# Optimization experiments

Hardware: AMD Instinct MI355X
Metric: run time of the kernel (lower is better)

## Reference

```python
import jax, jax.numpy as jnp
import numpy as np

LN2 = 0.6931471805599453

def ssp(x):
    # 'shifted_sp' activation: softplus(x) - log(2)
    return jax.nn.softplus(x) - LN2

def _res_chain(x, W1, b1, W2, b2):
    # PhysNetResidual chain: x <- lin2(ssp(lin1(ssp(x)))) + x
    # W1/W2: [n_res, F, F], b1/b2: [n_res, F]
    for j in range(W1.shape[0]):
        h = ssp(x) @ W1[j] + b1[j]
        x = ssp(h) @ W2[j] + b2[j] + x
    return x

def _physnet_module(feat, radial_aev, idx12, p):
    (W_I, b_I, W_J, b_J, W_gate, gvec, W_int, b_int,
     ri_W1, ri_b1, ri_W2, ri_b2,
     ra_W1, ra_b1, ra_W2, ra_b2,
     ro_W1, ro_b1, ro_W2, ro_b2, W_out, b_out) = p
    N, F = feat.shape
    # self term (no species are dummy -> non_dummy indexing is identity)
    h_self = ssp(ssp(feat) @ W_I + b_I)                       # [N,F]
    # pair messages
    gate = radial_aev @ W_gate                                 # [P,F] (no bias)
    f12 = feat[idx12]                                          # [2,P,F] gather
    fm = ssp(ssp(f12) @ W_J + b_J)                             # [2,P,F]
    pair_msg = gate[None] * fm                                 # [2,P,F]
    proto = jnp.zeros_like(feat).at[idx12.reshape(-1)].add(
        pair_msg.reshape(-1, F))                               # scatter-add
    proto = proto + h_self
    msg = _res_chain(proto, ri_W1, ri_b1, ri_W2, ri_b2)
    feat2 = feat * gvec + ssp(msg) @ W_int + b_int
    feat2 = _res_chain(feat2, ra_W1, ra_b1, ra_W2, ra_b2)
    e = ssp(_res_chain(feat2, ro_W1, ro_b1, ro_W2, ro_b2)) @ W_out + b_out  # [N]
    return e, feat2

def setup_inputs() -> dict:
    key = jax.random.key(0)
    L, F, R = 5, 128, 64
    M, A = 128, 64
    N = M * A
    P = 400000
    ks = jax.random.split(key, 20)
    s = 0.05  # small weight scale keeps activations stable across 5 modules
    inp = {
        'species': jax.random.randint(ks[0], (M, A), 0, 4, dtype=jnp.int32),
        'features': jax.random.normal(ks[1], (N, F), jnp.float32),
        'radial_aev': jax.random.uniform(ks[2], (P, R), jnp.float32),
        'atom_index12': jax.random.randint(ks[3], (2, P), 0, N, dtype=jnp.int32),
        'W_I': jax.random.normal(ks[4], (L, F, F)) * s,
        'b_I': jnp.zeros((L, F)),
        'W_J': jax.random.normal(ks[5], (L, F, F)) * s,
        'b_J': jnp.zeros((L, F)),
        'W_gate': jax.random.normal(ks[6], (L, R, F)) * s,
        'gvec': jnp.ones((L, F)),
        'W_int': jax.random.normal(ks[7], (L, F, F)) * s,
        'b_int': jnp.zeros((L, F)),
        'ri_W1': jax.random.normal(ks[8], (L, 3, F, F)) * s,
        'ri_b1': jnp.zeros((L, 3, F)),
        'ri_W2': jax.random.normal(ks[9], (L, 3, F, F)) * s,
        'ri_b2': jnp.zeros((L, 3, F)),
        'ra_W1': jax.random.normal(ks[10], (L, 2, F, F)) * s,
        'ra_b1': jnp.zeros((L, 2, F)),
        'ra_W2': jax.random.normal(ks[11], (L, 2, F, F)) * s,
        'ra_b2': jnp.zeros((L, 2, F)),
        'ro_W1': jax.random.normal(ks[12], (L, 1, F, F)) * s,
        'ro_b1': jnp.zeros((L, 1, F)),
        'ro_W2': jax.random.normal(ks[13], (L, 1, F, F)) * s,
        'ro_b2': jnp.zeros((L, 1, F)),
        'W_out': jax.random.normal(ks[14], (L, F)) * s,
        'b_out': jnp.zeros((L,)),
    }
    return inp

def reference(species, features, radial_aev, atom_index12,
              W_I, b_I, W_J, b_J, W_gate, gvec, W_int, b_int,
              ri_W1, ri_b1, ri_W2, ri_b2,
              ra_W1, ra_b1, ra_W2, ra_b2,
              ro_W1, ro_b1, ro_W2, ro_b2, W_out, b_out):
    M, A = species.shape
    params = (W_I, b_I, W_J, b_J, W_gate, gvec, W_int, b_int,
              ri_W1, ri_b1, ri_W2, ri_b2,
              ra_W1, ra_b1, ra_W2, ra_b2,
              ro_W1, ro_b1, ro_W2, ro_b2, W_out, b_out)
    feat = features
    energies = jnp.zeros((M * A,), features.dtype)
    for l in range(W_I.shape[0]):  # fixed small module loop
        p = tuple(arr[l] for arr in params)
        e, feat = _physnet_module(feat, radial_aev, atom_index12, p)
        energies = energies + e
    return energies.reshape(M, A), feat
```

## Files before the change

kernel.cpp:

```cpp
#include <hip/hip_runtime.h>


#define LN2F 0.69314718055994530942f
#define NB 128

using short8  = __attribute__((ext_vector_type(8))) short;
using float4v = __attribute__((ext_vector_type(4))) float;

__device__ __forceinline__ float sspf(float x) {
  float ax = fabsf(x);
  return fmaxf(x, 0.0f) + __logf(1.0f + __expf(-ax)) - LN2F;
}

__device__ __forceinline__ unsigned short f2bf(float x) {
  return (unsigned short)((__float_as_uint(x) + 0x8000u) >> 16);
}

__device__ __forceinline__ unsigned short f2bf_ne(float x) {
  unsigned int u = __float_as_uint(x);
  u += 0x7fffu + ((u >> 16) & 1u);
  return (unsigned short)(u >> 16);
}

struct K1Args {
  const float* wsrc[80];
  int isgate[80];
  const float* bp[17];
  int bstride[17];
  const float* b_out;
  const int* idx;
  unsigned short* Wt;
  float* bias_pack;
  unsigned int* H;
  int n2p, C;
};

__global__ __launch_bounds__(256) void k1_prep(K1Args K) {
  __shared__ unsigned int h[8192];
  int b = blockIdx.x, tid = threadIdx.x;
  if (b < 80) {
    const float* s = K.wsrc[b];
    unsigned short* d = K.Wt + (size_t)b * 16384;
    if (!K.isgate[b]) {
      for (int it = 0; it < 8; ++it) {
        int id = tid + it * 256;
        int lane = id & 63, mm = (id >> 6) & 3, c8 = id >> 8;
        int l16 = lane & 15, quad = lane >> 4;
        int n = 16 * c8 + l16, k0 = 8 * (4 * mm + quad);
        unsigned short tmp[8];
#pragma unroll
        for (int cc = 0; cc < 8; ++cc) tmp[cc] = f2bf_ne(s[(k0 + cc) * 128 + n]);
        *(uint4*)(d + c8 * 2048 + mm * 512 + lane * 8) = *(uint4*)tmp;
      }
    } else {
      for (int it = 0; it < 4; ++it) {
        int id = tid + it * 256;
        int lane = id & 63, mm = (id >> 6) & 1, c8 = id >> 7;
        int l16 = lane & 15, quad = lane >> 4;
        int n = 16 * c8 + l16, k0 = 8 * (4 * mm + quad);
        unsigned short tmp[8];
#pragma unroll
        for (int cc = 0; cc < 8; ++cc) tmp[cc] = f2bf_ne(s[(k0 + cc) * 128 + n]);
        *(uint4*)(d + c8 * 1024 + mm * 512 + lane * 8) = *(uint4*)tmp;
      }
    }
  } else if (b < 85) {
    int l = b - 80;
    for (int i = tid; i < 17 * 128; i += 256) {
      int s = i >> 7;
      K.bias_pack[(size_t)l * 2304 + i] = K.bp[s][l * K.bstride[s] + (i & 127)];
    }
    if (tid == 0) K.bias_pack[(size_t)l * 2304 + 17 * 128] = K.b_out[l];
  } else {
    int blk = b - 85;
    for (int i = tid; i < 8192; i += 256) h[i] = 0;
    __syncthreads();
    int s = blk * K.C, e = min(s + K.C, K.n2p);
    for (int i = s + tid; i < e; i += 256) atomicAdd(&h[K.idx[i]], 1u);
    __syncthreads();
    for (int i = tid; i < 8192; i += 256) K.H[(size_t)blk * 8192 + i] = h[i];
  }
}

__global__ __launch_bounds__(256) void col_scan(unsigned int* __restrict__ H,
                                                unsigned int* __restrict__ tot) {
  int a = blockIdx.x * 256 + threadIdx.x;
  unsigned int run = 0;
  for (int b = 0; b < NB; ++b) {
    unsigned int v = H[(size_t)b * 8192 + a];
    H[(size_t)b * 8192 + a] = run;
    run += v;
  }
  tot[a] = run;
}

__global__ __launch_bounds__(256) void place_pass(const int* __restrict__ idx,
                                                  const unsigned int* __restrict__ H,
                                                  const unsigned int* __restrict__ tot,
                                                  unsigned int* __restrict__ off_out,
                                                  unsigned int* __restrict__ pairid,
                                                  int P, int C) {
  __shared__ unsigned int pos[8192];
  __shared__ unsigned int wt4[4];
  int b = blockIdx.x, tid = threadIdx.x;
  unsigned int local[32], s = 0;
#pragma unroll
  for (int i = 0; i < 32; ++i) { local[i] = tot[tid * 32 + i]; s += local[i]; }
  unsigned int v = s;
  int lane = tid & 63, wv = tid >> 6;
#pragma unroll
  for (int o = 1; o < 64; o <<= 1) {
    unsigned int u = __shfl_up(v, o, 64);
    if (lane >= o) v += u;
  }
  if (lane == 63) wt4[wv] = v;
  __syncthreads();
  unsigned int base = 0;
  for (int k = 0; k < wv; ++k) base += wt4[k];
  unsigned int excl = base + v - s;
#pragma unroll
  for (int i = 0; i < 32; ++i) {
    pos[tid * 32 + i] = excl;
    if (b == 0) off_out[tid * 32 + i] = excl;
    excl += local[i];
  }
  if (b == 0 && tid == 255) off_out[8192] = excl;
  __syncthreads();
  for (int i = tid; i < 8192; i += 256) pos[i] += H[(size_t)b * 8192 + i];
  __syncthreads();
  int n2p = 2 * P;
  int s2 = b * C, e2 = min(s2 + C, n2p);
  for (int i = s2 + tid; i < e2; i += 256) {
    int a = idx[i];
    unsigned int p = atomicAdd(&pos[a], 1u);
    pairid[p] = (i >= P) ? (unsigned int)(i - P) : (unsigned int)i;
  }
}

__global__ __launch_bounds__(256) void gather_kernel(const float* __restrict__ radial,
                                                     const unsigned int* __restrict__ off,
                                                     const unsigned int* __restrict__ pairid,
                                                     float* __restrict__ S) {
  __shared__ float4v red[3][16];
  int a = blockIdx.x;
  int lane = threadIdx.x & 63, w = threadIdx.x >> 6;
  int grp = lane >> 4, l16v = lane & 15;
  unsigned int b = off[a], e = off[a + 1];
  float4v acc = {0.f, 0.f, 0.f, 0.f};
  for (unsigned int base = b; base < e; base += 128) {
    unsigned int pp[8];
#pragma unroll
    for (int k = 0; k < 8; ++k) {
      unsigned int j = base + k * 16 + w * 4 + grp;
      pp[k] = pairid[j < e ? j : b];
    }
    float4v vv[8];
#pragma unroll
    for (int k = 0; k < 8; ++k)
      vv[k] = *(const float4v*)(radial + (size_t)pp[k] * 64 + l16v * 4);
#pragma unroll
    for (int k = 0; k < 8; ++k) {
      unsigned int j = base + k * 16 + w * 4 + grp;
      if (j < e) acc += vv[k];
    }
  }
#pragma unroll
  for (int o = 16; o < 64; o <<= 1) {
#pragma unroll
    for (int cc = 0; cc < 4; ++cc) acc[cc] += __shfl_xor(acc[cc], o, 64);
  }
  if (w > 0 && grp == 0) red[w - 1][l16v] = acc;
  __syncthreads();
  if (w == 0 && grp == 0) {
    acc += red[0][l16v];
    acc += red[1][l16v];
    acc += red[2][l16v];
    *(float4v*)(S + (size_t)a * 64 + l16v * 4) = acc;
  }
}

struct ChainArgs {
  const float* feat_in;
  const float* S;
  const unsigned short* wt;
  const float* bias_pack;
  float* feat_out;
  float* energy;
};

#define MFMA_ __builtin_amdgcn_mfma_f32_16x16x32_bf16

#define BAR() { __builtin_amdgcn_sched_barrier(0); \
  asm volatile("s_waitcnt lgkmcnt(0)" ::: "memory"); \
  __builtin_amdgcn_s_barrier(); \
  __builtin_amdgcn_sched_barrier(0); }

#define LDW(WP, sp) { \
  const unsigned short* wp_ = (sp) + woff; \
  W[WP][0] = *(const short8*)(wp_); \
  W[WP][1] = *(const short8*)(wp_ + 512); \
  W[WP][2] = *(const short8*)(wp_ + 1024); \
  W[WP][3] = *(const short8*)(wp_ + 1536); }

#define G128R(AP, WP, ACC) { \
  short8 a0_ = *(const short8*)(aB + (AP)*4352); \
  short8 a1_ = *(const short8*)(aB + (AP)*4352 + 32); \
  short8 a2_ = *(const short8*)(aB + (AP)*4352 + 64); \
  short8 a3_ = *(const short8*)(aB + (AP)*4352 + 96); \
  ACC = MFMA_(a0_, W[WP][0], ACC, 0, 0, 0); \
  ACC = MFMA_(a1_, W[WP][1], ACC, 0, 0, 0); \
  ACC = MFMA_(a2_, W[WP][2], ACC, 0, 0, 0); \
  ACC = MFMA_(a3_, W[WP][3], ACC, 0, 0, 0); }

#define WSSPM(AP, V) { \
  wB[(AP)*4352]       = f2bf(sspf((V)[0])); \
  wB[(AP)*4352 + 136] = f2bf(sspf((V)[1])); \
  wB[(AP)*4352 + 272] = f2bf(sspf((V)[2])); \
  wB[(AP)*4352 + 408] = f2bf(sspf((V)[3])); }

#define MODBODY(L, S0) { \
  const float* bp = A.bias_pack + (L) * 2304; \
  const unsigned short* wtp = A.wt + (size_t)(L) * 16 * 16384; \
   \
  { float bv_ = bp[col0]; \
    LDW((S0)^1, wtp + 2*16384); \
    gG = Z; \
    { short8 s0_ = *(const short8*)(aS); short8 s1_ = *(const short8*)(aS + 32); \
      gG = MFMA_(s0_, GT0, gG, 0, 0, 0); \
      gG = MFMA_(s1_, GT1, gG, 0, 0, 0); } \
    fm = Z; G128R(0, (S0), fm); \
    for (int r = 0; r < 4; ++r) fm[r] = sspf(fm[r] + bv_); } \
   \
  { float bv_ = bp[128 + col0]; \
    LDW((S0), wtp + 3*16384); \
    if ((L) < 4) { \
      GT0 = *(const short8*)(wtp + 16*16384 + goff); \
      GT1 = *(const short8*)(wtp + 16*16384 + goff + 512); \
    } \
    t4 = Z; G128R(0, (S0)^1, t4); \
    for (int r = 0; r < 4; ++r) xf[r] = fm[r] * gG[r] + sspf(t4[r] + bv_); } \
  WSSPM(1, xf); BAR(); \
   \
  { float bv_ = bp[2*128 + col0]; LDW((S0)^1, wtp + 4*16384); \
    t4 = Z; G128R(1, (S0), t4); \
    for (int r = 0; r < 4; ++r) t4[r] += bv_; } \
  WSSPM(0, t4); BAR(); \
  { float bv_ = bp[3*128 + col0]; LDW((S0), wtp + 5*16384); \
    t4 = Z; G128R(0, (S0)^1, t4); \
    for (int r = 0; r < 4; ++r) xf[r] += t4[r] + bv_; } \
  WSSPM(1, xf); BAR(); \
  { float bv_ = bp[4*128 + col0]; LDW((S0)^1, wtp + 6*16384); \
    t4 = Z; G128R(1, (S0), t4); \
    for (int r = 0; r < 4; ++r) t4[r] += bv_; } \
  WSSPM(0, t4); BAR(); \
  { float bv_ = bp[5*128 + col0]; LDW((S0), wtp + 7*16384); \
    t4 = Z; G128R(0, (S0)^1, t4); \
    for (int r = 0; r < 4; ++r) xf[r] += t4[r] + bv_; } \
  WSSPM(1, xf); BAR(); \
  { float bv_ = bp[6*128 + col0]; LDW((S0)^1, wtp + 8*16384); \
    t4 = Z; G128R(1, (S0), t4); \
    for (int r = 0; r < 4; ++r) t4[r] += bv_; } \
  WSSPM(0, t4); BAR(); \
  { float bv_ = bp[7*128 + col0]; LDW((S0), wtp + 9*16384); \
    t4 = Z; G128R(0, (S0)^1, t4); \
    for (int r = 0; r < 4; ++r) xf[r] += t4[r] + bv_; } \
  WSSPM(1, xf); BAR(); \
   \
  { float bv_ = bp[8*128 + col0]; float gv_ = bp[15*128 + col0]; \
    LDW((S0)^1, wtp + 10*16384); \
    t4 = Z; G128R(1, (S0), t4); \
    for (int r = 0; r < 4; ++r) xf[r] = ff[r] * gv_ + t4[r] + bv_; } \
  WSSPM(0, xf); BAR(); \
   \
  { float bv_ = bp[9*128 + col0]; LDW((S0), wtp + 11*16384); \
    t4 = Z; G128R(0, (S0)^1, t4); \
    for (int r = 0; r < 4; ++r) t4[r] += bv_; } \
  WSSPM(1, t4); BAR(); \
  { float bv_ = bp[10*128 + col0]; LDW((S0)^1, wtp + 12*16384); \
    t4 = Z; G128R(1, (S0), t4); \
    for (int r = 0; r < 4; ++r) xf[r] += t4[r] + bv_; } \
  WSSPM(0, xf); BAR(); \
  { float bv_ = bp[11*128 + col0]; LDW((S0), wtp + 13*16384); \
    t4 = Z; G128R(0, (S0)^1, t4); \
    for (int r = 0; r < 4; ++r) t4[r] += bv_; } \
  WSSPM(1, t4); BAR(); \
  { float bv_ = bp[12*128 + col0]; LDW((S0)^1, wtp + 14*16384); \
    t4 = Z; G128R(1, (S0), t4); \
    for (int r = 0; r < 4; ++r) xf[r] += t4[r] + bv_; } \
  WSSPM(0, xf); BAR(); \
  ff = xf; \
  if ((L) == 4) { \
    for (int r = 0; r < 4; ++r) \
      A.feat_out[(size_t)(row0 + arow + quad*4 + r) * 128 + col0] = xf[r]; \
  } \
   \
  { float bv_ = bp[13*128 + col0]; LDW((S0), wtp + 15*16384); \
    t4 = Z; G128R(0, (S0)^1, t4); \
    for (int r = 0; r < 4; ++r) t4[r] += bv_; } \
  WSSPM(1, t4); BAR(); \
   \
  { float bv_ = bp[14*128 + col0]; float wv_ = bp[16*128 + col0]; \
    if ((L) < 4) LDW((S0)^1, wtp + 17*16384); \
    t4 = Z; G128R(1, (S0), t4); \
    p0 += sspf(xf[0] + t4[0] + bv_) * wv_; \
    p1 += sspf(xf[1] + t4[1] + bv_) * wv_; \
    p2 += sspf(xf[2] + t4[2] + bv_) * wv_; \
    p3 += sspf(xf[3] + t4[3] + bv_) * wv_; } \
  bsum += bp[17*128]; \
  BAR(); }

__global__ __launch_bounds__(1024, 4)
__attribute__((amdgpu_waves_per_eu(4, 4)))
void chain_kernel(ChainArgs A) {
  __shared__ __align__(16) unsigned short sA[2][32 * 136];
  __shared__ __align__(16) unsigned short sS[32 * 72];
  __shared__ float sE[32];

  const int tid  = threadIdx.x;
  const int row0 = blockIdx.x * 32;
  const int lane = tid & 63;
  const int w    = tid >> 6;
  const int g    = w >> 3;
  const int c    = w & 7;
  const int l16  = lane & 15;
  const int quad = lane >> 4;
  const int arow = 16 * g;
  const int col0 = 16 * c + l16;

  const int woff = c * 2048 + lane * 8;
  const int goff = c * 1024 + lane * 8;

  const unsigned short* aB = &sA[0][0] + (arow + l16) * 136 + quad * 8;
  unsigned short*       wB = &sA[0][0] + (arow + quad * 4) * 136 + col0;
  const unsigned short* aS = &sS[0] + (arow + l16) * 72 + quad * 8;

  short8 GT0, GT1;
  short8 W[2][4];
  GT0 = *(const short8*)(A.wt + goff);
  GT1 = *(const short8*)(A.wt + goff + 512);
  LDW(0, A.wt + 16384);

  for (int i = tid; i < 32 * 64; i += 1024) {
    int r = i >> 6, k = i & 63;
    sS[r * 72 + k] = f2bf(A.S[(size_t)(row0 + r) * 64 + k]);
  }
  for (int i = tid; i < 32 * 128; i += 1024) {
    int r = i >> 7, k = i & 127;
    sA[0][r * 136 + k] = f2bf(sspf(A.feat_in[(size_t)(row0 + r) * 128 + k]));
  }
  float4v ff;
#pragma unroll
  for (int r = 0; r < 4; ++r)
    ff[r] = A.feat_in[(size_t)(row0 + arow + quad * 4 + r) * 128 + col0];
  if (tid < 32) sE[tid] = 0.0f;
  __syncthreads();

  const float4v Z = {0.f, 0.f, 0.f, 0.f};
  float4v gG, fm, xf, t4;
  float p0 = 0.f, p1 = 0.f, p2 = 0.f, p3 = 0.f, bsum = 0.f;

  MODBODY(0, 0)
  MODBODY(1, 1)
  MODBODY(2, 0)
  MODBODY(3, 1)
  MODBODY(4, 0)

#pragma unroll
  for (int o = 1; o < 16; o <<= 1) {
    p0 += __shfl_xor(p0, o, 64);
    p1 += __shfl_xor(p1, o, 64);
    p2 += __shfl_xor(p2, o, 64);
    p3 += __shfl_xor(p3, o, 64);
  }
  if (l16 == 0) {
    atomicAdd(&sE[arow + quad * 4 + 0], p0);
    atomicAdd(&sE[arow + quad * 4 + 1], p1);
    atomicAdd(&sE[arow + quad * 4 + 2], p2);
    atomicAdd(&sE[arow + quad * 4 + 3], p3);
  }
  BAR();
  if (tid < 32) A.energy[row0 + tid] = sE[tid] + bsum;
}

extern "C" void kernel_launch(void* const* d_in, const int* in_sizes, int n_in,
                              void* d_out, int out_size, void* d_ws, size_t ws_size,
                              hipStream_t stream) {
  const float* features = (const float*)d_in[1];
  const float* radial   = (const float*)d_in[2];
  const int*   idx12    = (const int*)  d_in[3];
  const float* W_I    = (const float*)d_in[4];
  const float* b_I    = (const float*)d_in[5];
  const float* W_J    = (const float*)d_in[6];
  const float* b_J    = (const float*)d_in[7];
  const float* W_gate = (const float*)d_in[8];
  const float* gvec   = (const float*)d_in[9];
  const float* W_int  = (const float*)d_in[10];
  const float* b_int  = (const float*)d_in[11];
  const float* ri_W1  = (const float*)d_in[12];
  const float* ri_b1  = (const float*)d_in[13];
  const float* ri_W2  = (const float*)d_in[14];
  const float* ri_b2  = (const float*)d_in[15];
  const float* ra_W1  = (const float*)d_in[16];
  const float* ra_b1  = (const float*)d_in[17];
  const float* ra_W2  = (const float*)d_in[18];
  const float* ra_b2  = (const float*)d_in[19];
  const float* ro_W1  = (const float*)d_in[20];
  const float* ro_b1  = (const float*)d_in[21];
  const float* ro_W2  = (const float*)d_in[22];
  const float* ro_b2  = (const float*)d_in[23];
  const float* W_out  = (const float*)d_in[24];
  const float* b_out  = (const float*)d_in[25];

  const int N = in_sizes[1] / 128;
  const int P = in_sizes[3] / 2;
  const int L = in_sizes[25];
  const int n2p = 2 * P;
  const int C = (n2p + NB - 1) / NB;

  float* S = (float*)d_ws;
  float* bias_pack = S + (size_t)N * 64;
  unsigned short* Wt = (unsigned short*)(bias_pack + 5 * 2304);
  unsigned int* H      = (unsigned int*)(Wt + (size_t)80 * 16384);
  unsigned int* tot    = H + (size_t)NB * 8192;
  unsigned int* off    = tot + N;
  unsigned int* pairid = off + N + 4;

  K1Args k1;
  for (int l = 0; l < L; ++l) {
    const float* fx[16] = {
      W_gate + l * 8192,
      W_J + l * 16384, W_I + l * 16384,
      ri_W1 + (l * 3 + 0) * 16384, ri_W2 + (l * 3 + 0) * 16384,
      ri_W1 + (l * 3 + 1) * 16384, ri_W2 + (l * 3 + 1) * 16384,
      ri_W1 + (l * 3 + 2) * 16384, ri_W2 + (l * 3 + 2) * 16384,
      W_int + l * 16384,
      ra_W1 + (l * 2 + 0) * 16384, ra_W2 + (l * 2 + 0) * 16384,
      ra_W1 + (l * 2 + 1) * 16384, ra_W2 + (l * 2 + 1) * 16384,
      ro_W1 + l * 16384, ro_W2 + l * 16384 };
    for (int t = 0; t < 16; ++t) { k1.wsrc[l * 16 + t] = fx[t]; k1.isgate[l * 16 + t] = (t == 0); }
  }
  const float* bp[17] = { b_J, b_I,
    ri_b1, ri_b2, ri_b1 + 128, ri_b2 + 128, ri_b1 + 256, ri_b2 + 256,
    b_int, ra_b1, ra_b2, ra_b1 + 128, ra_b2 + 128, ro_b1, ro_b2, gvec, W_out };
  int st[17] = {128,128, 384,384,384,384,384,384, 128, 256,256,256,256, 128,128,128,128};
  for (int q = 0; q < 17; ++q) { k1.bp[q] = bp[q]; k1.bstride[q] = st[q]; }
  k1.b_out = b_out;
  k1.idx = idx12; k1.Wt = Wt; k1.bias_pack = bias_pack; k1.H = H;
  k1.n2p = n2p; k1.C = C;
  k1_prep<<<80 + 5 + NB, 256, 0, stream>>>(k1);

  col_scan<<<32, 256, 0, stream>>>(H, tot);
  place_pass<<<NB, 256, 0, stream>>>(idx12, H, tot, off, pairid, P, C);
  gather_kernel<<<N, 256, 0, stream>>>(radial, off, pairid, S);

  ChainArgs ca;
  ca.feat_in   = features;
  ca.S         = S;
  ca.wt        = Wt;
  ca.bias_pack = bias_pack;
  ca.energy    = (float*)d_out;
  ca.feat_out  = (float*)d_out + N;
  chain_kernel<<<N / 32, 1024, 0, stream>>>(ca);
}
```

Before: 324.1 us.

## Shrink chain kernel blocks to 16 rows and preload biases into MFMA accumulators

The chain kernel now processes 16 atoms per block with 512 threads (8 waves, one per column slice) instead of 32 atoms with 1024 threads. This doubles the grid size and reduces how many waves must reach each barrier. Each wave now loads the full weight set for fewer rows, so per-row weight traffic doubles. Biases for each module are also loaded once into registers and used to initialise the MFMA accumulators, which removes the separate bias adds. That raises register pressure.

Measured after the change: 320.8 us. No clear change (-1.0%).

```diff
diff --git a/kernel.cpp b/kernel.cpp
--- a/kernel.cpp
+++ b/kernel.cpp
@@ -189,6 +189,7 @@
 };
 
 #define MFMA_ __builtin_amdgcn_mfma_f32_16x16x32_bf16
+#define APOFF 2176
 
 #define BAR() { __builtin_amdgcn_sched_barrier(0); \
   asm volatile("s_waitcnt lgkmcnt(0)" ::: "memory"); \
@@ -202,137 +203,118 @@
   W[WP][2] = *(const short8*)(wp_ + 1024); \
   W[WP][3] = *(const short8*)(wp_ + 1536); }
 
+#define BINI(ACC, B) { (ACC)[0] = (B); (ACC)[1] = (B); (ACC)[2] = (B); (ACC)[3] = (B); }
+
 #define G128R(AP, WP, ACC) { \
-  short8 a0_ = *(const short8*)(aB + (AP)*4352); \
-  short8 a1_ = *(const short8*)(aB + (AP)*4352 + 32); \
-  short8 a2_ = *(const short8*)(aB + (AP)*4352 + 64); \
-  short8 a3_ = *(const short8*)(aB + (AP)*4352 + 96); \
+  short8 a0_ = *(const short8*)(aB + (AP)*APOFF); \
+  short8 a1_ = *(const short8*)(aB + (AP)*APOFF + 32); \
+  short8 a2_ = *(const short8*)(aB + (AP)*APOFF + 64); \
+  short8 a3_ = *(const short8*)(aB + (AP)*APOFF + 96); \
   ACC = MFMA_(a0_, W[WP][0], ACC, 0, 0, 0); \
   ACC = MFMA_(a1_, W[WP][1], ACC, 0, 0, 0); \
   ACC = MFMA_(a2_, W[WP][2], ACC, 0, 0, 0); \
   ACC = MFMA_(a3_, W[WP][3], ACC, 0, 0, 0); }
 
 #define WSSPM(AP, V) { \
-  wB[(AP)*4352]       = f2bf(sspf((V)[0])); \
-  wB[(AP)*4352 + 136] = f2bf(sspf((V)[1])); \
-  wB[(AP)*4352 + 272] = f2bf(sspf((V)[2])); \
-  wB[(AP)*4352 + 408] = f2bf(sspf((V)[3])); }
+  wB[(AP)*APOFF]       = f2bf(sspf((V)[0])); \
+  wB[(AP)*APOFF + 136] = f2bf(sspf((V)[1])); \
+  wB[(AP)*APOFF + 272] = f2bf(sspf((V)[2])); \
+  wB[(AP)*APOFF + 408] = f2bf(sspf((V)[3])); }
 
 #define MODBODY(L, S0) { \
   const float* bp = A.bias_pack + (L) * 2304; \
   const unsigned short* wtp = A.wt + (size_t)(L) * 16 * 16384; \
-   \
-  { float bv_ = bp[col0]; \
-    LDW((S0)^1, wtp + 2*16384); \
+  float bW[15]; \
+  _Pragma("unroll") \
+  for (int q = 0; q < 15; ++q) bW[q] = bp[q * 128 + col0]; \
+  float gvv = bp[15 * 128 + col0], wvv = bp[16 * 128 + col0]; \
+   \
+  { LDW((S0)^1, wtp + 2*16384); \
     gG = Z; \
     { short8 s0_ = *(const short8*)(aS); short8 s1_ = *(const short8*)(aS + 32); \
       gG = MFMA_(s0_, GT0, gG, 0, 0, 0); \
       gG = MFMA_(s1_, GT1, gG, 0, 0, 0); } \
-    fm = Z; G128R(0, (S0), fm); \
-    for (int r = 0; r < 4; ++r) fm[r] = sspf(fm[r] + bv_); } \
-   \
-  { float bv_ = bp[128 + col0]; \
-    LDW((S0), wtp + 3*16384); \
+    BINI(fm, bW[0]); G128R(0, (S0), fm); \
+    for (int r = 0; r < 4; ++r) fm[r] = sspf(fm[r]); } \
+   \
+  { LDW((S0), wtp + 3*16384); \
     if ((L) < 4) { \
       GT0 = *(const short8*)(wtp + 16*16384 + goff); \
       GT1 = *(const short8*)(wtp + 16*16384 + goff + 512); \
     } \
-    t4 = Z; G128R(0, (S0)^1, t4); \
-    for (int r = 0; r < 4; ++r) xf[r] = fm[r] * gG[r] + sspf(t4[r] + bv_); } \
+    BINI(t4, bW[1]); G128R(0, (S0)^1, t4); \
+    for (int r = 0; r < 4; ++r) xf[r] = fm[r] * gG[r] + sspf(t4[r]); } \
   WSSPM(1, xf); BAR(); \
    \
-  { float bv_ = bp[2*128 + col0]; LDW((S0)^1, wtp + 4*16384); \
-    t4 = Z; G128R(1, (S0), t4); \
-    for (int r = 0; r < 4; ++r) t4[r] += bv_; } \
+  { LDW((S0)^1, wtp + 4*16384); BINI(t4, bW[2]); G128R(1, (S0), t4); } \
   WSSPM(0, t4); BAR(); \
-  { float bv_ = bp[3*128 + col0]; LDW((S0), wtp + 5*16384); \
-    t4 = Z; G128R(0, (S0)^1, t4); \
-    for (int r = 0; r < 4; ++r) xf[r] += t4[r] + bv_; } \
+  { LDW((S0), wtp + 5*16384); BINI(t4, bW[3]); G128R(0, (S0)^1, t4); \
+    for (int r = 0; r < 4; ++r) xf[r] += t4[r]; } \
   WSSPM(1, xf); BAR(); \
-  { float bv_ = bp[4*128 + col0]; LDW((S0)^1, wtp + 6*16384); \
-    t4 = Z; G128R(1, (S0), t4); \
-    for (int r = 0; r < 4; ++r) t4[r] += bv_; } \
+  { LDW((S0)^1, wtp + 6*16384); BINI(t4, bW[4]); G128R(1, (S0), t4); } \
   WSSPM(0, t4); BAR(); \
-  { float bv_ = bp[5*128 + col0]; LDW((S0), wtp + 7*16384); \
-    t4 = Z; G128R(0, (S0)^1, t4); \
-    for (int r = 0; r < 4; ++r) xf[r] += t4[r] + bv_; } \
+  { LDW((S0), wtp + 7*16384); BINI(t4, bW[5]); G128R(0, (S0)^1, t4); \
+    for (int r = 0; r < 4; ++r) xf[r] += t4[r]; } \
   WSSPM(1, xf); BAR(); \
-  { float bv_ = bp[6*128 + col0]; LDW((S0)^1, wtp + 8*16384); \
-    t4 = Z; G128R(1, (S0), t4); \
-    for (int r = 0; r < 4; ++r) t4[r] += bv_; } \
+  { LDW((S0)^1, wtp + 8*16384); BINI(t4, bW[6]); G128R(1, (S0), t4); } \
   WSSPM(0, t4); BAR(); \
-  { float bv_ = bp[7*128 + col0]; LDW((S0), wtp + 9*16384); \
-    t4 = Z; G128R(0, (S0)^1, t4); \
-    for (int r = 0; r < 4; ++r) xf[r] += t4[r] + bv_; } \
+  { LDW((S0), wtp + 9*16384); BINI(t4, bW[7]); G128R(0, (S0)^1, t4); \
+    for (int r = 0; r < 4; ++r) xf[r] += t4[r]; } \
   WSSPM(1, xf); BAR(); \
    \
-  { float bv_ = bp[8*128 + col0]; float gv_ = bp[15*128 + col0]; \
-    LDW((S0)^1, wtp + 10*16384); \
-    t4 = Z; G128R(1, (S0), t4); \
-    for (int r = 0; r < 4; ++r) xf[r] = ff[r] * gv_ + t4[r] + bv_; } \
+  { LDW((S0)^1, wtp + 10*16384); BINI(t4, bW[8]); G128R(1, (S0), t4); \
+    for (int r = 0; r < 4; ++r) xf[r] = ff[r] * gvv + t4[r]; } \
   WSSPM(0, xf); BAR(); \
    \
-  { float bv_ = bp[9*128 + col0]; LDW((S0), wtp + 11*16384); \
-    t4 = Z; G128R(0, (S0)^1, t4); \
-    for (int r = 0; r < 4; ++r) t4[r] += bv_; } \
+  { LDW((S0), wtp + 11*16384); BINI(t4, bW[9]); G128R(0, (S0)^1, t4); } \
   WSSPM(1, t4); BAR(); \
-  { float bv_ = bp[10*128 + col0]; LDW((S0)^1, wtp + 12*16384); \
-    t4 = Z; G128R(1, (S0), t4); \
-    for (int r = 0; r < 4; ++r) xf[r] += t4[r] + bv_; } \
+  { LDW((S0)^1, wtp + 12*16384); BINI(t4, bW[10]); G128R(1, (S0), t4); \
+    for (int r = 0; r < 4; ++r) xf[r] += t4[r]; } \
   WSSPM(0, xf); BAR(); \
-  { float bv_ = bp[11*128 + col0]; LDW((S0), wtp + 13*16384); \
-    t4 = Z; G128R(0, (S0)^1, t4); \
-    for (int r = 0; r < 4; ++r) t4[r] += bv_; } \
+  { LDW((S0), wtp + 13*16384); BINI(t4, bW[11]); G128R(0, (S0)^1, t4); } \
   WSSPM(1, t4); BAR(); \
-  { float bv_ = bp[12*128 + col0]; LDW((S0)^1, wtp + 14*16384); \
-    t4 = Z; G128R(1, (S0), t4); \
-    for (int r = 0; r < 4; ++r) xf[r] += t4[r] + bv_; } \
+  { LDW((S0)^1, wtp + 14*16384); BINI(t4, bW[12]); G128R(1, (S0), t4); \
+    for (int r = 0; r < 4; ++r) xf[r] += t4[r]; } \
   WSSPM(0, xf); BAR(); \
   ff = xf; \
   if ((L) == 4) { \
     for (int r = 0; r < 4; ++r) \
-      A.feat_out[(size_t)(row0 + arow + quad*4 + r) * 128 + col0] = xf[r]; \
+      A.feat_out[(size_t)(row0 + quad*4 + r) * 128 + col0] = xf[r]; \
   } \
    \
-  { float bv_ = bp[13*128 + col0]; LDW((S0), wtp + 15*16384); \
-    t4 = Z; G128R(0, (S0)^1, t4); \
-    for (int r = 0; r < 4; ++r) t4[r] += bv_; } \
+  { LDW((S0), wtp + 15*16384); BINI(t4, bW[13]); G128R(0, (S0)^1, t4); } \
   WSSPM(1, t4); BAR(); \
    \
-  { float bv_ = bp[14*128 + col0]; float wv_ = bp[16*128 + col0]; \
-    if ((L) < 4) LDW((S0)^1, wtp + 17*16384); \
-    t4 = Z; G128R(1, (S0), t4); \
-    p0 += sspf(xf[0] + t4[0] + bv_) * wv_; \
-    p1 += sspf(xf[1] + t4[1] + bv_) * wv_; \
-    p2 += sspf(xf[2] + t4[2] + bv_) * wv_; \
-    p3 += sspf(xf[3] + t4[3] + bv_) * wv_; } \
+  { if ((L) < 4) LDW((S0)^1, wtp + 17*16384); \
+    BINI(t4, bW[14]); G128R(1, (S0), t4); \
+    p0 += sspf(xf[0] + t4[0]) * wvv; \
+    p1 += sspf(xf[1] + t4[1]) * wvv; \
+    p2 += sspf(xf[2] + t4[2]) * wvv; \
+    p3 += sspf(xf[3] + t4[3]) * wvv; } \
   bsum += bp[17*128]; \
   BAR(); }
 
-__global__ __launch_bounds__(1024, 4)
+__global__ __launch_bounds__(512)
 __attribute__((amdgpu_waves_per_eu(4, 4)))
 void chain_kernel(ChainArgs A) {
-  __shared__ __align__(16) unsigned short sA[2][32 * 136];
-  __shared__ __align__(16) unsigned short sS[32 * 72];
-  __shared__ float sE[32];
+  __shared__ __align__(16) unsigned short sA[2][16 * 136];
+  __shared__ __align__(16) unsigned short sS[16 * 72];
+  __shared__ float sE[16];
 
   const int tid  = threadIdx.x;
-  const int row0 = blockIdx.x * 32;
+  const int row0 = blockIdx.x * 16;
   const int lane = tid & 63;
-  const int w    = tid >> 6;
-  const int g    = w >> 3;
-  const int c    = w & 7;
+  const int c    = tid >> 6;
   const int l16  = lane & 15;
   const int quad = lane >> 4;
-  const int arow = 16 * g;
   const int col0 = 16 * c + l16;
 
   const int woff = c * 2048 + lane * 8;
   const int goff = c * 1024 + lane * 8;
 
-  const unsigned short* aB = &sA[0][0] + (arow + l16) * 136 + quad * 8;
-  unsigned short*       wB = &sA[0][0] + (arow + quad * 4) * 136 + col0;
-  const unsigned short* aS = &sS[0] + (arow + l16) * 72 + quad * 8;
+  const unsigned short* aB = &sA[0][0] + l16 * 136 + quad * 8;
+  unsigned short*       wB = &sA[0][0] + (quad * 4) * 136 + col0;
+  const unsigned short* aS = &sS[0] + l16 * 72 + quad * 8;
 
   short8 GT0, GT1;
   short8 W[2][4];
@@ -340,19 +322,19 @@
   GT1 = *(const short8*)(A.wt + goff + 512);
   LDW(0, A.wt + 16384);
 
-  for (int i = tid; i < 32 * 64; i += 1024) {
+  for (int i = tid; i < 16 * 64; i += 512) {
     int r = i >> 6, k = i & 63;
     sS[r * 72 + k] = f2bf(A.S[(size_t)(row0 + r) * 64 + k]);
   }
-  for (int i = tid; i < 32 * 128; i += 1024) {
+  for (int i = tid; i < 16 * 128; i += 512) {
     int r = i >> 7, k = i & 127;
     sA[0][r * 136 + k] = f2bf(sspf(A.feat_in[(size_t)(row0 + r) * 128 + k]));
   }
   float4v ff;
 #pragma unroll
   for (int r = 0; r < 4; ++r)
-    ff[r] = A.feat_in[(size_t)(row0 + arow + quad * 4 + r) * 128 + col0];
-  if (tid < 32) sE[tid] = 0.0f;
+    ff[r] = A.feat_in[(size_t)(row0 + quad * 4 + r) * 128 + col0];
+  if (tid < 16) sE[tid] = 0.0f;
   __syncthreads();
 
   const float4v Z = {0.f, 0.f, 0.f, 0.f};
@@ -373,13 +355,13 @@
     p3 += __shfl_xor(p3, o, 64);
   }
   if (l16 == 0) {
-    atomicAdd(&sE[arow + quad * 4 + 0], p0);
-    atomicAdd(&sE[arow + quad * 4 + 1], p1);
-    atomicAdd(&sE[arow + quad * 4 + 2], p2);
-    atomicAdd(&sE[arow + quad * 4 + 3], p3);
+    atomicAdd(&sE[quad * 4 + 0], p0);
+    atomicAdd(&sE[quad * 4 + 1], p1);
+    atomicAdd(&sE[quad * 4 + 2], p2);
+    atomicAdd(&sE[quad * 4 + 3], p3);
   }
   BAR();
-  if (tid < 32) A.energy[row0 + tid] = sE[tid] + bsum;
+  if (tid < 16) A.energy[row0 + tid] = sE[tid] + bsum;
 }
 
 extern "C" void kernel_launch(void* const* d_in, const int* in_sizes, int n_in,
@@ -460,5 +442,5 @@
   ca.bias_pack = bias_pack;
   ca.energy    = (float*)d_out;
   ca.feat_out  = (float*)d_out + N;
-  chain_kernel<<<N / 32, 1024, 0, stream>>>(ca);
-}
+  chain_kernel<<<N / 16, 512, 0, stream>>>(ca);
+}
```
